# Kernel optimization log

Hardware: AMD Instinct MI355X
Metric: run time of the kernel (lower is better)

The kernel has to match this reference:

```python
import jax, jax.numpy as jnp
import numpy as np


def setup_inputs() -> dict:
    key = jax.random.key(0)
    ks = jax.random.split(key, 10)
    NT, NB = 64, 1024          # (ntime, nbatch) leading dims from nested vmap(vmap(...))
    NS = 6                     # nsize = 1 + ninternal
    NI = NS + 2                # input features = nsize + 2 (erate, T)
    H = 256                    # hidden width
    dt = jnp.float32
    inp = {
        "t": jax.random.normal(ks[0], (NT, NB), dt),
        "y": jax.random.normal(ks[1], (NT, NB, NS), dt),
        "erate": jax.random.normal(ks[2], (NT, NB), dt),
        "T": jax.random.normal(ks[3], (NT, NB), dt),
        # He-style scaling so ReLU activations stay well-conditioned
        "w1": jax.random.normal(ks[4], (H, NI), dt) / np.sqrt(NI).astype(np.float32),
        "w2": jax.random.normal(ks[5], (H, H), dt) / np.sqrt(H).astype(np.float32),
        "w3": jax.random.normal(ks[6], (NS, H), dt) / np.sqrt(H).astype(np.float32),
        "b1": jax.random.normal(ks[7], (H,), dt) * 0.1,
        "b2": jax.random.normal(ks[8], (H,), dt) * 0.1,
        "b3": jax.random.normal(ks[9], (NS,), dt) * 0.1,
    }
    return inp


def reference(t, y, erate, T, w1, w2, w3, b1, b2, b3):
    # rate(): 3-layer ReLU MLP on x = [y, erate, T]
    x = jnp.concatenate([y, erate[..., None], T[..., None]], axis=-1)  # (...,NI)
    z1 = jnp.einsum('ij,...j->...i', w1, x) + b1                       # (...,H)
    v1 = jax.nn.relu(z1)
    z2 = jnp.einsum('ij,...j->...i', w2, v1) + b2                      # (...,H)
    v2 = jax.nn.relu(z2)
    ydot = jnp.einsum('ij,...j->...i', w3, v2) + b3                    # (...,NS)

    # Analytic Jacobians, identical math to vmap(vmap(jacfwd(rate))):
    # J = w3 @ diag(m2) @ w2 @ diag(m1) @ w1, with m = relu'(z) = (z>0)
    m1 = (z1 > 0).astype(x.dtype)
    m2 = (z2 > 0).astype(x.dtype)
    A = w3 * m2[..., None, :]                                          # (...,NS,H)
    B = jnp.einsum('...ih,hj->...ij', A, w2) * m1[..., None, :]        # (...,NS,H)
    J = jnp.einsum('...ih,hj->...ij', B, w1)                           # (...,NS,NI)

    nsize = y.shape[-1]
    dydot_dy = J[..., :nsize]          # (...,NS,NS)
    dydot_de = J[..., nsize]           # (...,NS)
    dydot_dT = J[..., nsize + 1]       # (...,NS)
    return (ydot, dydot_dy, dydot_de, dydot_dT)
```

## Files before the change

### kernel.cpp

```cpp
#include <hip/hip_runtime.h>
#include <hip/hip_bf16.h>


typedef unsigned short ushort_t;
typedef __attribute__((ext_vector_type(8))) short bf16x8;
typedef __attribute__((ext_vector_type(4))) float f32x4;

#define NSAMP (64 * 1024)
#define NG16 (NSAMP / 16)
#define OFF_YDOT 0
#define OFF_DY (NSAMP * 6)
#define OFF_DE (OFF_DY + NSAMP * 36)
#define OFF_DT (OFF_DE + NSAMP * 6)

__device__ __align__(16) ushort_t g_w2T_hi[65536];
__device__ __align__(16) ushort_t g_w2T_mid[65536];
__device__ __align__(16) ushort_t g_w2T_lo[65536];
__device__ __align__(16) ushort_t g_w2B[65536];
__device__ __align__(16) ushort_t g_w1e[4096];
__device__ __align__(16) ushort_t g_w3b[1536];

static __device__ __forceinline__ ushort_t f2bf(float f) {
    union { __hip_bfloat16 b; ushort_t u; } c;
    c.b = __float2bfloat16(f);
    return c.u;
}
static __device__ __forceinline__ float bf2f(ushort_t u) {
    union { ushort_t u; __hip_bfloat16 b; } c;
    c.u = u;
    return __bfloat162float(c.b);
}

static __device__ __forceinline__ int swzu(int E) { return E ^ ((E >> 3) & 0x30); }
static __device__ __forceinline__ int swzo(int o) { return o ^ ((o >> 3) & 0x6); }

__global__ void prep_kernel(const float* __restrict__ w1, const float* __restrict__ w2,
                            const float* __restrict__ w3) {
    const int gtid = blockIdx.x * blockDim.x + threadIdx.x;
    const int stride = gridDim.x * blockDim.x;
    for (int idx = gtid; idx < 65536; idx += stride) {
        const int nt = idx >> 12, kt = (idx >> 9) & 7, L = (idx >> 3) & 63, jj = idx & 7;
        const int n = nt * 16 + (L & 15);
        const int k = kt * 32 + ((L >> 4) & 3) * 8 + jj;
        const float vT = w2[n * 256 + k];
        const ushort_t hi = f2bf(vT);
        const float r1 = vT - bf2f(hi);
        const ushort_t mid = f2bf(r1);
        g_w2T_hi[idx]  = hi;
        g_w2T_mid[idx] = mid;
        g_w2T_lo[idx]  = f2bf(r1 - bf2f(mid));
        g_w2B[idx] = f2bf(w2[k * 256 + n]);
    }
    for (int idx = gtid; idx < 4096; idx += stride) {
        const int kt = idx >> 9, L = (idx >> 3) & 63, jj = idx & 7;
        const int kout = L & 15;
        const int j = kt * 32 + ((L >> 4) & 3) * 8 + jj;
        g_w1e[idx] = (kout < 8) ? f2bf(w1[j * 8 + kout]) : (ushort_t)0;
    }
    for (int idx = gtid; idx < 1536; idx += stride) g_w3b[idx] = f2bf(w3[idx]);
}

#define SMEM_BYTES 40960

__global__ __launch_bounds__(256, 3) void fused_kernel(
    const float* __restrict__ y, const float* __restrict__ erate,
    const float* __restrict__ Tin, const float* __restrict__ w1,
    const float* __restrict__ b1, const float* __restrict__ b2,
    const float* __restrict__ b3, float* __restrict__ out)
{
    __shared__ __align__(16) char smem[SMEM_BYTES];
    ushort_t* v1hi  = (ushort_t*)(smem + 0);
    float*    Jsh   = (float*)(smem + 0);
    float*    ydsh  = (float*)(smem + 1536);
    ushort_t* v1mid = (ushort_t*)(smem + 8192);
    ushort_t* v1lo  = (ushort_t*)(smem + 16384);
    ushort_t* A2    = (ushort_t*)(smem + 8192);
    float*    xs    = (float*)(smem + 24576);
    ushort_t* v2B   = (ushort_t*)(smem + 32768);

    const int tid  = threadIdx.x;
    const int lane = tid & 63;
    const int wave = tid >> 6;
    const int l15  = lane & 15;
    const int quad = lane >> 4;

    float w1r[8];
#pragma unroll
    for (int k = 0; k < 8; ++k) w1r[k] = w1[tid * 8 + k];
    const float b1r = b1[tid];
    float b2v[4];
#pragma unroll
    for (int n = 0; n < 4; ++n) b2v[n] = b2[(wave * 4 + n) * 16 + l15];

    const int g = blockIdx.x;
    const int s0 = g * 16;

    if (tid < 128) {
        const int s = tid >> 3, k = tid & 7;
        float v;
        if (k < 6)       v = y[(s0 + s) * 6 + k];
        else if (k == 6) v = erate[s0 + s];
        else             v = Tin[s0 + s];
        xs[s * 8 + k] = v;
    }
    __syncthreads();

    unsigned int m1self = 0;
    {
        const int ktw = tid >> 5, qd = (tid >> 3) & 3, jj = tid & 7;
#pragma unroll 4
        for (int s = 0; s < 16; ++s) {
            float z = b1r;
#pragma unroll
            for (int k = 0; k < 8; ++k) z = fmaf(w1r[k], xs[s * 8 + k], z);
            const float v = fmaxf(z, 0.0f);
            m1self |= (v > 0.0f ? 1u : 0u) << s;
            const ushort_t hi = f2bf(v);
            const float r1 = v - bf2f(hi);
            const ushort_t mid = f2bf(r1);
            const int e = swzu((ktw * 64 + (s | (qd << 4))) * 8 + jj);
            v1hi[e]  = hi;
            v1mid[e] = mid;
            v1lo[e]  = f2bf(r1 - bf2f(mid));
        }
    }
    __syncthreads();

    {
        f32x4 cz[4];
#pragma unroll
        for (int n = 0; n < 4; ++n) cz[n] = (f32x4){0, 0, 0, 0};
#pragma unroll 2
        for (int kt = 0; kt < 8; ++kt) {
            const int ao = swzo(kt * 64 + lane) * 8;
            bf16x8 ahi = *(const bf16x8*)&v1hi[ao];
            bf16x8 ami = *(const bf16x8*)&v1mid[ao];
            bf16x8 alo = *(const bf16x8*)&v1lo[ao];
#pragma unroll
            for (int n = 0; n < 4; ++n) {
                const int bidx = (((wave * 4 + n) * 8 + kt) * 64 + lane) * 8;
                bf16x8 bh = *(const bf16x8*)&g_w2T_hi[bidx];
                bf16x8 bm = *(const bf16x8*)&g_w2T_mid[bidx];
                bf16x8 bl = *(const bf16x8*)&g_w2T_lo[bidx];
                __builtin_amdgcn_s_setprio(1);
                cz[n] = __builtin_amdgcn_mfma_f32_16x16x32_bf16(alo, bh, cz[n], 0, 0, 0);
                cz[n] = __builtin_amdgcn_mfma_f32_16x16x32_bf16(ami, bm, cz[n], 0, 0, 0);
                cz[n] = __builtin_amdgcn_mfma_f32_16x16x32_bf16(ahi, bl, cz[n], 0, 0, 0);
                cz[n] = __builtin_amdgcn_mfma_f32_16x16x32_bf16(ami, bh, cz[n], 0, 0, 0);
                cz[n] = __builtin_amdgcn_mfma_f32_16x16x32_bf16(ahi, bm, cz[n], 0, 0, 0);
                cz[n] = __builtin_amdgcn_mfma_f32_16x16x32_bf16(ahi, bh, cz[n], 0, 0, 0);
                __builtin_amdgcn_s_setprio(0);
            }
        }
#pragma unroll
        for (int n = 0; n < 4; ++n) {
            const int h = (wave * 4 + n) * 16 + l15;
            const int ktd = h >> 5, qd = (h >> 3) & 3, jj = h & 7;
#pragma unroll
            for (int r = 0; r < 4; ++r) {
                const int s = quad * 4 + r;
                const float v2 = fmaxf(cz[n][r] + b2v[n], 0.0f);
                v2B[swzu((ktd * 64 + (s | (qd << 4))) * 8 + jj)] = f2bf(v2);
            }
        }
    }
    __syncthreads();

#pragma unroll 1
    for (int c = 0; c < 2; ++c) {
        if (tid < 192) {
            const int mt = tid >> 6;
            const int m = mt * 16 + l15;
            const int sl = m / 6, i = m - sl * 6;
            const int sg = c * 8 + sl;
#pragma unroll 2
            for (int kt = 0; kt < 8; ++kt) {
                bf16x8 vv = *(const bf16x8*)&v2B[swzo(kt * 64 + (sg | (quad << 4))) * 8];
                bf16x8 wv = *(const bf16x8*)&g_w3b[i * 256 + kt * 32 + quad * 8];
                bf16x8 o;
#pragma unroll
                for (int e = 0; e < 8; ++e)
                    o[e] = ((ushort_t)vv[e] != 0) ? wv[e] : (short)0;
                *(bf16x8*)&A2[swzo((mt * 8 + kt) * 64 + lane) * 8] = o;
            }
        }
        __syncthreads();

        if (wave == 3) {
            f32x4 cy[3];
#pragma unroll
            for (int mt = 0; mt < 3; ++mt) cy[mt] = (f32x4){0, 0, 0, 0};
#pragma unroll 2
            for (int kt = 0; kt < 8; ++kt) {
                bf16x8 bv = *(const bf16x8*)&v2B[swzo(kt * 64 + lane) * 8];
                __builtin_amdgcn_s_setprio(1);
#pragma unroll
                for (int mt = 0; mt < 3; ++mt) {
                    bf16x8 a = *(const bf16x8*)&A2[swzo((mt * 8 + kt) * 64 + lane) * 8];
                    cy[mt] = __builtin_amdgcn_mfma_f32_16x16x32_bf16(a, bv, cy[mt], 0, 0, 0);
                }
                __builtin_amdgcn_s_setprio(0);
            }
#pragma unroll
            for (int mt = 0; mt < 3; ++mt) {
#pragma unroll
                for (int r = 0; r < 4; ++r) {
                    const int m = mt * 16 + quad * 4 + r;
                    const int sl = m / 6, i = m - sl * 6;
                    if (l15 == c * 8 + sl) ydsh[m] = cy[mt][r] + b3[i];
                }
            }
        }

        f32x4 cc[3][4];
#pragma unroll
        for (int mt = 0; mt < 3; ++mt)
#pragma unroll
            for (int n = 0; n < 4; ++n) cc[mt][n] = (f32x4){0, 0, 0, 0};
#pragma unroll 2
        for (int kt = 0; kt < 8; ++kt) {
            bf16x8 a[3];
#pragma unroll
            for (int mt = 0; mt < 3; ++mt)
                a[mt] = *(const bf16x8*)&A2[swzo((mt * 8 + kt) * 64 + lane) * 8];
#pragma unroll
            for (int n = 0; n < 4; ++n) {
                bf16x8 b = *(const bf16x8*)&g_w2B[(((wave * 4 + n) * 8 + kt) * 64 + lane) * 8];
                __builtin_amdgcn_s_setprio(1);
#pragma unroll
                for (int mt = 0; mt < 3; ++mt)
                    cc[mt][n] = __builtin_amdgcn_mfma_f32_16x16x32_bf16(a[mt], b, cc[mt][n], 0, 0, 0);
                __builtin_amdgcn_s_setprio(0);
            }
        }
        __syncthreads();

#pragma unroll
        for (int n = 0; n < 4; ++n) {
            const unsigned int mcol = (unsigned int)__shfl((int)m1self, n * 16 + l15, 64);
            const int j = (wave * 4 + n) * 16 + l15;
            const int ktd = j >> 5, qd = (j >> 3) & 3, jjd = j & 7;
#pragma unroll
            for (int mt = 0; mt < 3; ++mt) {
#pragma unroll
                for (int r = 0; r < 4; ++r) {
                    const int m = mt * 16 + quad * 4 + r;
                    const int sg = c * 8 + m / 6;
                    const ushort_t bm =
                        ((mcol >> sg) & 1u) ? f2bf(cc[mt][n][r]) : (ushort_t)0;
                    A2[swzu(((mt * 8 + ktd) * 64 + ((m & 15) | (qd << 4))) * 8 + jjd)] = bm;
                }
            }
        }
        __syncthreads();

        if (wave < 3) {
            f32x4 dc = {0, 0, 0, 0};
#pragma unroll 2
            for (int kt = 0; kt < 8; ++kt) {
                bf16x8 a = *(const bf16x8*)&A2[swzo((wave * 8 + kt) * 64 + lane) * 8];
                bf16x8 b = *(const bf16x8*)&g_w1e[(kt * 64 + lane) * 8];
                dc = __builtin_amdgcn_mfma_f32_16x16x32_bf16(a, b, dc, 0, 0, 0);
            }
            if (l15 < 8) {
#pragma unroll
                for (int r = 0; r < 4; ++r) {
                    const int m = wave * 16 + quad * 4 + r;
                    Jsh[m * 8 + l15] = dc[r];
                }
            }
        }
        __syncthreads();

        {
            const int s0c = s0 + c * 8;
            const long base6 = (long)s0c * 6;
            {
                const int u = tid;
                const int s = u / 36, rem = u - s * 36, ii = rem / 6, jy = rem - ii * 6;
                out[OFF_DY + (long)s0c * 36 + u] = Jsh[(s * 6 + ii) * 8 + jy];
            }
            if (tid < 32) {
                const int u = 256 + tid;
                const int s = u / 36, rem = u - s * 36, ii = rem / 6, jy = rem - ii * 6;
                out[OFF_DY + (long)s0c * 36 + u] = Jsh[(s * 6 + ii) * 8 + jy];
            }
            if (tid < 48) out[OFF_YDOT + base6 + tid] = ydsh[tid];
            const int t2 = tid - 64;
            if (t2 >= 0 && t2 < 48) out[OFF_DE + base6 + t2] = Jsh[t2 * 8 + 6];
            const int t3 = tid - 128;
            if (t3 >= 0 && t3 < 48) out[OFF_DT + base6 + t3] = Jsh[t3 * 8 + 7];
        }
    }
}

extern "C" void kernel_launch(void* const* d_in, const int* in_sizes, int n_in,
                              void* d_out, int out_size, void* d_ws, size_t ws_size,
                              hipStream_t stream) {
    const float* y     = (const float*)d_in[1];
    const float* erate = (const float*)d_in[2];
    const float* Tin   = (const float*)d_in[3];
    const float* w1    = (const float*)d_in[4];
    const float* w2    = (const float*)d_in[5];
    const float* w3    = (const float*)d_in[6];
    const float* b1    = (const float*)d_in[7];
    const float* b2    = (const float*)d_in[8];
    const float* b3    = (const float*)d_in[9];
    float* out = (float*)d_out;

    prep_kernel<<<dim3(64), dim3(256), 0, stream>>>(w1, w2, w3);
    fused_kernel<<<dim3(NG16), dim3(256), 0, stream>>>(
        y, erate, Tin, w1, b1, b2, b3, out);
}
```

Measured before the change: 282.0 us.

## Process 32 samples per 512-thread block to reuse weight fragments across two sample groups

Each block now handles two 16-sample groups with 8 waves. Each wave covers half as many hidden-column tiles, and every w2 fragment loaded from global memory feeds MFMAs for both groups, which halves weight traffic per sample. The relu mask is moved from a register shuffle into shared memory. Shared memory grows to about 72KB per block, which may reduce occupancy, and the tail stages still leave one of every four waves idle.

After: 270.2 us. 1.04x faster.

```diff
diff --git a/kernel.cpp b/kernel.cpp
--- a/kernel.cpp
+++ b/kernel.cpp
@@ -7,7 +7,7 @@
 typedef __attribute__((ext_vector_type(4))) float f32x4;
 
 #define NSAMP (64 * 1024)
-#define NG16 (NSAMP / 16)
+#define NG32 (NSAMP / 32)
 #define OFF_YDOT 0
 #define OFF_DY (NSAMP * 6)
 #define OFF_DE (OFF_DY + NSAMP * 36)
@@ -60,9 +60,9 @@
     for (int idx = gtid; idx < 1536; idx += stride) g_w3b[idx] = f2bf(w3[idx]);
 }
 
-#define SMEM_BYTES 40960
-
-__global__ __launch_bounds__(256, 3) void fused_kernel(
+#define SMEM_BYTES 72064
+
+__global__ __launch_bounds__(512, 4) void fused_kernel(
     const float* __restrict__ y, const float* __restrict__ erate,
     const float* __restrict__ Tin, const float* __restrict__ w1,
     const float* __restrict__ b1, const float* __restrict__ b2,
@@ -70,32 +70,37 @@
 {
     __shared__ __align__(16) char smem[SMEM_BYTES];
     ushort_t* v1hi  = (ushort_t*)(smem + 0);
-    float*    Jsh   = (float*)(smem + 0);
-    float*    ydsh  = (float*)(smem + 1536);
-    ushort_t* v1mid = (ushort_t*)(smem + 8192);
-    ushort_t* v1lo  = (ushort_t*)(smem + 16384);
-    ushort_t* A2    = (ushort_t*)(smem + 8192);
-    float*    xs    = (float*)(smem + 24576);
-    ushort_t* v2B   = (ushort_t*)(smem + 32768);
+    ushort_t* v1mid = (ushort_t*)(smem + 16384);
+    ushort_t* v1lo  = (ushort_t*)(smem + 32768);
+    ushort_t* A2    = (ushort_t*)(smem + 0);
+    float*    xs    = (float*)(smem + 49152);
+    ushort_t* v2B   = (ushort_t*)(smem + 50176);
+    float*    Jsh   = (float*)(smem + 66560);
+    float*    ydsh  = (float*)(smem + 69632);
+    unsigned int* m1sh = (unsigned int*)(smem + 70016);
 
     const int tid  = threadIdx.x;
     const int lane = tid & 63;
     const int wave = tid >> 6;
+    const int wg   = wave >> 2;
+    const int w4   = wave & 3;
     const int l15  = lane & 15;
     const int quad = lane >> 4;
+    const int jz   = tid & 255;
+    const int gz   = tid >> 8;
 
     float w1r[8];
 #pragma unroll
-    for (int k = 0; k < 8; ++k) w1r[k] = w1[tid * 8 + k];
-    const float b1r = b1[tid];
-    float b2v[4];
-#pragma unroll
-    for (int n = 0; n < 4; ++n) b2v[n] = b2[(wave * 4 + n) * 16 + l15];
+    for (int k = 0; k < 8; ++k) w1r[k] = w1[jz * 8 + k];
+    const float b1r = b1[jz];
+    float b2v[2];
+#pragma unroll
+    for (int n = 0; n < 2; ++n) b2v[n] = b2[(wave * 2 + n) * 16 + l15];
 
     const int g = blockIdx.x;
-    const int s0 = g * 16;
-
-    if (tid < 128) {
+    const int s0 = g * 32;
+
+    if (tid < 256) {
         const int s = tid >> 3, k = tid & 7;
         float v;
         if (k < 6)       v = y[(s0 + s) * 6 + k];
@@ -105,62 +110,76 @@
     }
     __syncthreads();
 
-    unsigned int m1self = 0;
     {
-        const int ktw = tid >> 5, qd = (tid >> 3) & 3, jj = tid & 7;
+        unsigned int m1self = 0;
+        const int ktw = jz >> 5, qd = (jz >> 3) & 3, jj = jz & 7;
+        const int vb = gz * 4096;
 #pragma unroll 4
         for (int s = 0; s < 16; ++s) {
             float z = b1r;
 #pragma unroll
-            for (int k = 0; k < 8; ++k) z = fmaf(w1r[k], xs[s * 8 + k], z);
+            for (int k = 0; k < 8; ++k) z = fmaf(w1r[k], xs[(gz * 16 + s) * 8 + k], z);
             const float v = fmaxf(z, 0.0f);
             m1self |= (v > 0.0f ? 1u : 0u) << s;
             const ushort_t hi = f2bf(v);
             const float r1 = v - bf2f(hi);
             const ushort_t mid = f2bf(r1);
-            const int e = swzu((ktw * 64 + (s | (qd << 4))) * 8 + jj);
+            const int e = vb + swzu((ktw * 64 + (s | (qd << 4))) * 8 + jj);
             v1hi[e]  = hi;
             v1mid[e] = mid;
             v1lo[e]  = f2bf(r1 - bf2f(mid));
         }
+        m1sh[tid] = m1self;
     }
     __syncthreads();
 
     {
-        f32x4 cz[4];
-#pragma unroll
-        for (int n = 0; n < 4; ++n) cz[n] = (f32x4){0, 0, 0, 0};
+        f32x4 cz[2][2];
+#pragma unroll
+        for (int gi = 0; gi < 2; ++gi)
+#pragma unroll
+            for (int n = 0; n < 2; ++n) cz[gi][n] = (f32x4){0, 0, 0, 0};
 #pragma unroll 2
         for (int kt = 0; kt < 8; ++kt) {
             const int ao = swzo(kt * 64 + lane) * 8;
-            bf16x8 ahi = *(const bf16x8*)&v1hi[ao];
-            bf16x8 ami = *(const bf16x8*)&v1mid[ao];
-            bf16x8 alo = *(const bf16x8*)&v1lo[ao];
-#pragma unroll
-            for (int n = 0; n < 4; ++n) {
-                const int bidx = (((wave * 4 + n) * 8 + kt) * 64 + lane) * 8;
+            bf16x8 ahi[2], ami[2], alo[2];
+#pragma unroll
+            for (int gi = 0; gi < 2; ++gi) {
+                ahi[gi] = *(const bf16x8*)&v1hi[gi * 4096 + ao];
+                ami[gi] = *(const bf16x8*)&v1mid[gi * 4096 + ao];
+                alo[gi] = *(const bf16x8*)&v1lo[gi * 4096 + ao];
+            }
+#pragma unroll
+            for (int n = 0; n < 2; ++n) {
+                const int bidx = (((wave * 2 + n) * 8 + kt) * 64 + lane) * 8;
                 bf16x8 bh = *(const bf16x8*)&g_w2T_hi[bidx];
                 bf16x8 bm = *(const bf16x8*)&g_w2T_mid[bidx];
                 bf16x8 bl = *(const bf16x8*)&g_w2T_lo[bidx];
                 __builtin_amdgcn_s_setprio(1);
-                cz[n] = __builtin_amdgcn_mfma_f32_16x16x32_bf16(alo, bh, cz[n], 0, 0, 0);
-                cz[n] = __builtin_amdgcn_mfma_f32_16x16x32_bf16(ami, bm, cz[n], 0, 0, 0);
-                cz[n] = __builtin_amdgcn_mfma_f32_16x16x32_bf16(ahi, bl, cz[n], 0, 0, 0);
-                cz[n] = __builtin_amdgcn_mfma_f32_16x16x32_bf16(ami, bh, cz[n], 0, 0, 0);
-                cz[n] = __builtin_amdgcn_mfma_f32_16x16x32_bf16(ahi, bm, cz[n], 0, 0, 0);
-                cz[n] = __builtin_amdgcn_mfma_f32_16x16x32_bf16(ahi, bh, cz[n], 0, 0, 0);
+#pragma unroll
+                for (int gi = 0; gi < 2; ++gi) {
+                    cz[gi][n] = __builtin_amdgcn_mfma_f32_16x16x32_bf16(alo[gi], bh, cz[gi][n], 0, 0, 0);
+                    cz[gi][n] = __builtin_amdgcn_mfma_f32_16x16x32_bf16(ami[gi], bm, cz[gi][n], 0, 0, 0);
+                    cz[gi][n] = __builtin_amdgcn_mfma_f32_16x16x32_bf16(ahi[gi], bl, cz[gi][n], 0, 0, 0);
+                    cz[gi][n] = __builtin_amdgcn_mfma_f32_16x16x32_bf16(ami[gi], bh, cz[gi][n], 0, 0, 0);
+                    cz[gi][n] = __builtin_amdgcn_mfma_f32_16x16x32_bf16(ahi[gi], bm, cz[gi][n], 0, 0, 0);
+                    cz[gi][n] = __builtin_amdgcn_mfma_f32_16x16x32_bf16(ahi[gi], bh, cz[gi][n], 0, 0, 0);
+                }
                 __builtin_amdgcn_s_setprio(0);
             }
         }
 #pragma unroll
-        for (int n = 0; n < 4; ++n) {
-            const int h = (wave * 4 + n) * 16 + l15;
+        for (int n = 0; n < 2; ++n) {
+            const int h = (wave * 2 + n) * 16 + l15;
             const int ktd = h >> 5, qd = (h >> 3) & 3, jj = h & 7;
 #pragma unroll
-            for (int r = 0; r < 4; ++r) {
-                const int s = quad * 4 + r;
-                const float v2 = fmaxf(cz[n][r] + b2v[n], 0.0f);
-                v2B[swzu((ktd * 64 + (s | (qd << 4))) * 8 + jj)] = f2bf(v2);
+            for (int gi = 0; gi < 2; ++gi) {
+#pragma unroll
+                for (int r = 0; r < 4; ++r) {
+                    const int s = quad * 4 + r;
+                    const float v2 = fmaxf(cz[gi][n][r] + b2v[n], 0.0f);
+                    v2B[gi * 4096 + swzu((ktd * 64 + (s | (qd << 4))) * 8 + jj)] = f2bf(v2);
+                }
             }
         }
     }
@@ -168,35 +187,35 @@
 
 #pragma unroll 1
     for (int c = 0; c < 2; ++c) {
-        if (tid < 192) {
-            const int mt = tid >> 6;
+        if (w4 < 3) {
+            const int mt = w4;
             const int m = mt * 16 + l15;
             const int sl = m / 6, i = m - sl * 6;
             const int sg = c * 8 + sl;
 #pragma unroll 2
             for (int kt = 0; kt < 8; ++kt) {
-                bf16x8 vv = *(const bf16x8*)&v2B[swzo(kt * 64 + (sg | (quad << 4))) * 8];
+                bf16x8 vv = *(const bf16x8*)&v2B[wg * 4096 + swzo(kt * 64 + (sg | (quad << 4))) * 8];
                 bf16x8 wv = *(const bf16x8*)&g_w3b[i * 256 + kt * 32 + quad * 8];
                 bf16x8 o;
 #pragma unroll
                 for (int e = 0; e < 8; ++e)
                     o[e] = ((ushort_t)vv[e] != 0) ? wv[e] : (short)0;
-                *(bf16x8*)&A2[swzo((mt * 8 + kt) * 64 + lane) * 8] = o;
+                *(bf16x8*)&A2[wg * 12288 + swzo((mt * 8 + kt) * 64 + lane) * 8] = o;
             }
         }
         __syncthreads();
 
-        if (wave == 3) {
+        if (w4 == 3) {
             f32x4 cy[3];
 #pragma unroll
             for (int mt = 0; mt < 3; ++mt) cy[mt] = (f32x4){0, 0, 0, 0};
 #pragma unroll 2
             for (int kt = 0; kt < 8; ++kt) {
-                bf16x8 bv = *(const bf16x8*)&v2B[swzo(kt * 64 + lane) * 8];
+                bf16x8 bv = *(const bf16x8*)&v2B[wg * 4096 + swzo(kt * 64 + lane) * 8];
                 __builtin_amdgcn_s_setprio(1);
 #pragma unroll
                 for (int mt = 0; mt < 3; ++mt) {
-                    bf16x8 a = *(const bf16x8*)&A2[swzo((mt * 8 + kt) * 64 + lane) * 8];
+                    bf16x8 a = *(const bf16x8*)&A2[wg * 12288 + swzo((mt * 8 + kt) * 64 + lane) * 8];
                     cy[mt] = __builtin_amdgcn_mfma_f32_16x16x32_bf16(a, bv, cy[mt], 0, 0, 0);
                 }
                 __builtin_amdgcn_s_setprio(0);
@@ -207,89 +226,99 @@
                 for (int r = 0; r < 4; ++r) {
                     const int m = mt * 16 + quad * 4 + r;
                     const int sl = m / 6, i = m - sl * 6;
-                    if (l15 == c * 8 + sl) ydsh[m] = cy[mt][r] + b3[i];
-                }
-            }
-        }
-
-        f32x4 cc[3][4];
-#pragma unroll
-        for (int mt = 0; mt < 3; ++mt)
-#pragma unroll
-            for (int n = 0; n < 4; ++n) cc[mt][n] = (f32x4){0, 0, 0, 0};
+                    if (l15 == c * 8 + sl) ydsh[wg * 48 + m] = cy[mt][r] + b3[i];
+                }
+            }
+        }
+
+        f32x4 cc[2][3][2];
+#pragma unroll
+        for (int gi = 0; gi < 2; ++gi)
+#pragma unroll
+            for (int mt = 0; mt < 3; ++mt)
+#pragma unroll
+                for (int n = 0; n < 2; ++n) cc[gi][mt][n] = (f32x4){0, 0, 0, 0};
 #pragma unroll 2
         for (int kt = 0; kt < 8; ++kt) {
-            bf16x8 a[3];
-#pragma unroll
-            for (int mt = 0; mt < 3; ++mt)
-                a[mt] = *(const bf16x8*)&A2[swzo((mt * 8 + kt) * 64 + lane) * 8];
-#pragma unroll
-            for (int n = 0; n < 4; ++n) {
-                bf16x8 b = *(const bf16x8*)&g_w2B[(((wave * 4 + n) * 8 + kt) * 64 + lane) * 8];
+            bf16x8 a[2][3];
+#pragma unroll
+            for (int gi = 0; gi < 2; ++gi)
+#pragma unroll
+                for (int mt = 0; mt < 3; ++mt)
+                    a[gi][mt] = *(const bf16x8*)&A2[gi * 12288 + swzo((mt * 8 + kt) * 64 + lane) * 8];
+#pragma unroll
+            for (int n = 0; n < 2; ++n) {
+                bf16x8 b = *(const bf16x8*)&g_w2B[(((wave * 2 + n) * 8 + kt) * 64 + lane) * 8];
                 __builtin_amdgcn_s_setprio(1);
 #pragma unroll
-                for (int mt = 0; mt < 3; ++mt)
-                    cc[mt][n] = __builtin_amdgcn_mfma_f32_16x16x32_bf16(a[mt], b, cc[mt][n], 0, 0, 0);
+                for (int gi = 0; gi < 2; ++gi)
+#pragma unroll
+                    for (int mt = 0; mt < 3; ++mt)
+                        cc[gi][mt][n] = __builtin_amdgcn_mfma_f32_16x16x32_bf16(a[gi][mt], b, cc[gi][mt][n], 0, 0, 0);
                 __builtin_amdgcn_s_setprio(0);
             }
         }
         __syncthreads();
 
 #pragma unroll
-        for (int n = 0; n < 4; ++n) {
-            const unsigned int mcol = (unsigned int)__shfl((int)m1self, n * 16 + l15, 64);
-            const int j = (wave * 4 + n) * 16 + l15;
-            const int ktd = j >> 5, qd = (j >> 3) & 3, jjd = j & 7;
-#pragma unroll
-            for (int mt = 0; mt < 3; ++mt) {
-#pragma unroll
-                for (int r = 0; r < 4; ++r) {
-                    const int m = mt * 16 + quad * 4 + r;
-                    const int sg = c * 8 + m / 6;
-                    const ushort_t bm =
-                        ((mcol >> sg) & 1u) ? f2bf(cc[mt][n][r]) : (ushort_t)0;
-                    A2[swzu(((mt * 8 + ktd) * 64 + ((m & 15) | (qd << 4))) * 8 + jjd)] = bm;
+        for (int gi = 0; gi < 2; ++gi) {
+#pragma unroll
+            for (int n = 0; n < 2; ++n) {
+                const int j = (wave * 2 + n) * 16 + l15;
+                const unsigned int mcol = m1sh[gi * 256 + j];
+                const int ktd = j >> 5, qd = (j >> 3) & 3, jjd = j & 7;
+#pragma unroll
+                for (int mt = 0; mt < 3; ++mt) {
+#pragma unroll
+                    for (int r = 0; r < 4; ++r) {
+                        const int m = mt * 16 + quad * 4 + r;
+                        const int sg = c * 8 + m / 6;
+                        const ushort_t bm =
+                            ((mcol >> sg) & 1u) ? f2bf(cc[gi][mt][n][r]) : (ushort_t)0;
+                        A2[gi * 12288 + swzu(((mt * 8 + ktd) * 64 + ((m & 15) | (qd << 4))) * 8 + jjd)] = bm;
+                    }
                 }
             }
         }
         __syncthreads();
 
-        if (wave < 3) {
+        if (w4 < 3) {
             f32x4 dc = {0, 0, 0, 0};
 #pragma unroll 2
             for (int kt = 0; kt < 8; ++kt) {
-                bf16x8 a = *(const bf16x8*)&A2[swzo((wave * 8 + kt) * 64 + lane) * 8];
+                bf16x8 a = *(const bf16x8*)&A2[wg * 12288 + swzo((w4 * 8 + kt) * 64 + lane) * 8];
                 bf16x8 b = *(const bf16x8*)&g_w1e[(kt * 64 + lane) * 8];
                 dc = __builtin_amdgcn_mfma_f32_16x16x32_bf16(a, b, dc, 0, 0, 0);
             }
             if (l15 < 8) {
 #pragma unroll
                 for (int r = 0; r < 4; ++r) {
-                    const int m = wave * 16 + quad * 4 + r;
-                    Jsh[m * 8 + l15] = dc[r];
+                    const int m = w4 * 16 + quad * 4 + r;
+                    Jsh[(wg * 48 + m) * 8 + l15] = dc[r];
                 }
             }
         }
         __syncthreads();
 
         {
-            const int s0c = s0 + c * 8;
+            const int tg = tid & 255;
+            const int s0c = s0 + gz * 16 + c * 8;
             const long base6 = (long)s0c * 6;
             {
-                const int u = tid;
+                const int u = tg;
                 const int s = u / 36, rem = u - s * 36, ii = rem / 6, jy = rem - ii * 6;
-                out[OFF_DY + (long)s0c * 36 + u] = Jsh[(s * 6 + ii) * 8 + jy];
-            }
-            if (tid < 32) {
-                const int u = 256 + tid;
+                out[OFF_DY + (long)s0c * 36 + u] = Jsh[(gz * 48 + s * 6 + ii) * 8 + jy];
+            }
+            if (tg < 32) {
+                const int u = 256 + tg;
                 const int s = u / 36, rem = u - s * 36, ii = rem / 6, jy = rem - ii * 6;
-                out[OFF_DY + (long)s0c * 36 + u] = Jsh[(s * 6 + ii) * 8 + jy];
-            }
-            if (tid < 48) out[OFF_YDOT + base6 + tid] = ydsh[tid];
-            const int t2 = tid - 64;
-            if (t2 >= 0 && t2 < 48) out[OFF_DE + base6 + t2] = Jsh[t2 * 8 + 6];
-            const int t3 = tid - 128;
-            if (t3 >= 0 && t3 < 48) out[OFF_DT + base6 + t3] = Jsh[t3 * 8 + 7];
+                out[OFF_DY + (long)s0c * 36 + u] = Jsh[(gz * 48 + s * 6 + ii) * 8 + jy];
+            }
+            if (tg < 48) out[OFF_YDOT + base6 + tg] = ydsh[gz * 48 + tg];
+            const int t2 = tg - 64;
+            if (t2 >= 0 && t2 < 48) out[OFF_DE + base6 + t2] = Jsh[(gz * 48 + t2) * 8 + 6];
+            const int t3 = tg - 128;
+            if (t3 >= 0 && t3 < 48) out[OFF_DT + base6 + t3] = Jsh[(gz * 48 + t3) * 8 + 7];
         }
     }
 }
@@ -309,6 +338,6 @@
     float* out = (float*)d_out;
 
     prep_kernel<<<dim3(64), dim3(256), 0, stream>>>(w1, w2, w3);
-    fused_kernel<<<dim3(NG16), dim3(256), 0, stream>>>(
+    fused_kernel<<<dim3(NG32), dim3(512), 0, stream>>>(
         y, erate, Tin, w1, b1, b2, b3, out);
 }
```
